# Optimization experiments

Hardware: AMD Instinct MI355X
Metric: run time of the kernel (lower is better)

Reference implementation:

```python
import jax, jax.numpy as jnp
import numpy as np

# Fuzzy system constants (from _init_fuzzy_system)
X1_C = jnp.arange(5.0)                 # x1 gauss centers 0,1,2,3,4 ; sigma 1
X2_C = jnp.arange(5.0) * 45.0          # x2 gauss centers 0,45,90,135,180 ; sigma 45
OUT_C = jnp.array([-0.3, 0.1, 0.5, 0.9, 1.3], dtype=jnp.float32)  # consequent centers ; sigma 0.3
Z = jnp.asarray(np.arange(-0.3, 1.31, 0.01), dtype=jnp.float32)   # 161-pt output universe

# Mamdani rules: list per consequent level of (x1_level, x2_level) OR-terms, levels XS..XL = 0..4
RULES = [
    [(2, 4), (3, 4), (3, 3), (4, 3), (4, 4)],            # -> coupling XS
    [(1, 4), (2, 3), (3, 2), (4, 1)],                    # -> S
    [(0, 4), (1, 3), (2, 2), (3, 1), (4, 0)],            # -> M
    [(0, 3), (1, 2), (2, 1), (3, 0)],                    # -> L
    [(0, 2), (0, 1), (0, 0), (1, 1), (1, 0), (2, 0)],    # -> XL
]


def gauss(x, c, s):
    return jnp.exp(-0.5 * ((x - c) / s) ** 2)


def setup_inputs() -> dict:
    key = jax.random.key(0)
    k1, k2, k3, k4 = jax.random.split(key, 4)
    N, E, D = 50000, 1000000, 8
    h = jax.random.normal(k1, (N, D), dtype=jnp.float32)
    src_idx = jax.random.randint(k2, (E,), 0, N, dtype=jnp.int32)
    dst_idx = jax.random.randint(k3, (E,), 0, N, dtype=jnp.int32)
    etypes = jax.random.randint(k4, (E,), 0, 3, dtype=jnp.int32)
    return {"h": h, "src_idx": src_idx, "dst_idx": dst_idx, "etypes": etypes}


def reference(h, src_idx, dst_idx, etypes):
    # edge vector: dst['h'] - src['h']
    v = h[dst_idx] - h[src_idx]                       # [E, D]
    # Ante_generator: x1 = |v| (distance, clipped to universe), x2 = angle(v, e1) in degrees
    n = jnp.sqrt(jnp.sum(v * v, axis=-1) + 1e-12)     # [E]
    x1 = jnp.clip(n, 0.0, 4.0)
    cosang = jnp.clip(v[:, 0] / n, -0.999999, 0.999999)
    x2 = jnp.degrees(jnp.arccos(cosang))              # [E] in [0, 180]
    # antecedent memberships
    mu1 = gauss(x1[:, None], X1_C[None, :], 1.0)      # [E, 5]
    mu2 = gauss(x2[:, None], X2_C[None, :], 45.0)     # [E, 5]
    zmf = gauss(Z[None, :], OUT_C[:, None], 0.3)      # [5, 161]
    # Mamdani: rule activation = max over OR-terms of min(mu1, mu2);
    # implication = min(act, consequent mf); aggregation = max over rules
    agg = jnp.zeros((x1.shape[0], Z.shape[0]), dtype=h.dtype)  # [E, 161]
    for r, pairs in enumerate(RULES):
        act = jnp.max(
            jnp.stack([jnp.minimum(mu1[:, i], mu2[:, j]) for i, j in pairs], axis=-1),
            axis=-1,
        )                                             # [E]
        agg = jnp.maximum(agg, jnp.minimum(act[:, None], zmf[r][None, :]))
    # centroid defuzzification
    coupling_degree = jnp.sum(agg * Z[None, :], axis=-1) / jnp.sum(agg, axis=-1)
    return coupling_degree
```

## Files before the change

kernel.cpp:

```cpp
#include <hip/hip_runtime.h>

static constexpr double cexp_taylor(double x) {
    double s = 1.0, t = 1.0;
    for (int i = 1; i < 40; ++i) { t = t * x / (double)i; s += t; }
    return s;
}
static constexpr double cpow_int(double b, long e) {
    double r = 1.0, p = b;
    while (e > 0) { if (e & 1) r *= p; p *= p; e >>= 1; }
    return r;
}
struct ZmfTab { float v[5][161]; };
static constexpr ZmfTab make_zmf() {
    ZmfTab t{};
    const double c0 = cexp_taylor(-1.0 / 1800.0);
    for (int r = 0; r < 5; ++r)
        for (int k = 0; k < 161; ++k) {
            long d = (long)(k - 40 * r);
            t.v[r][k] = (float)cpow_int(c0, d * d);
        }
    return t;
}
static constexpr ZmfTab ZMF = make_zmf();
static constexpr float ZCUT = 1e-4f;

__device__ __forceinline__ float fuzzy_F(float x1, float u)
{
    float m1[5], m2[5];
#pragma unroll
    for (int i = 0; i < 5; ++i) {
        float d1 = x1 - (float)i;
        float d2 = u  - (float)i;
        m1[i] = __expf(-0.5f * d1 * d1);
        m2[i] = __expf(-0.5f * d2 * d2);
    }

    float a0 = fmaxf(fmaxf(fminf(m1[2], m2[4]), fminf(m1[3], m2[4])),
               fmaxf(fminf(m1[3], m2[3]),
               fmaxf(fminf(m1[4], m2[3]), fminf(m1[4], m2[4]))));
    float a1 = fmaxf(fmaxf(fminf(m1[1], m2[4]), fminf(m1[2], m2[3])),
               fmaxf(fminf(m1[3], m2[2]), fminf(m1[4], m2[1])));
    float a2 = fmaxf(fmaxf(fminf(m1[0], m2[4]), fminf(m1[1], m2[3])),
               fmaxf(fminf(m1[2], m2[2]),
               fmaxf(fminf(m1[3], m2[1]), fminf(m1[4], m2[0]))));
    float a3 = fmaxf(fmaxf(fminf(m1[0], m2[3]), fminf(m1[1], m2[2])),
               fmaxf(fminf(m1[2], m2[1]), fminf(m1[3], m2[0])));
    float a4 = fmaxf(fmaxf(fmaxf(fminf(m1[0], m2[2]), fminf(m1[0], m2[1])),
               fmaxf(fminf(m1[0], m2[0]), fminf(m1[1], m2[1]))),
               fmaxf(fminf(m1[1], m2[0]), fminf(m1[2], m2[0])));
    float a[5] = {a0, a1, a2, a3, a4};

    float s0 = 0.0f, s1 = 0.0f;
#pragma unroll
    for (int k = 0; k < 161; ++k) {
        float m = -1.0f;
        bool first = true;
#pragma unroll
        for (int r = 0; r < 5; ++r) {
            if (ZMF.v[r][k] >= ZCUT) {
                float tmin = fminf(a[r], ZMF.v[r][k]);
                m = first ? tmin : fmaxf(m, tmin);
                first = false;
            }
        }
        s0 += m;
        s1 = fmaf(m, (float)k, s1);
    }
    return fmaf(0.01f, s1 / s0, -0.3f);
}

#define GN 256

__global__ __launch_bounds__(256) void build_table_kernel(float2* __restrict__ tab2)
{
    int idx = blockIdx.x * blockDim.x + threadIdx.x;
    int i1 = idx >> 8;
    int i2 = idx & 255;
    const float h = 4.0f / 255.0f;
    float f = fuzzy_F((float)i1 * h, (float)i2 * h);
    tab2[idx].x = f;
    if (i2 > 0)   tab2[idx - 1].y = f;
    if (i2 == 255) tab2[idx].y = f;
}

__device__ __forceinline__ float edge_eval(
    const float4* __restrict__ h4, const float2* __restrict__ tab2,
    int si, int di)
{
    float4 sa = h4[2 * si], sb = h4[2 * si + 1];
    float4 da = h4[2 * di], db = h4[2 * di + 1];

    float v0 = da.x - sa.x, v1 = da.y - sa.y, v2 = da.z - sa.z, v3 = da.w - sa.w;
    float v4 = db.x - sb.x, v5 = db.y - sb.y, v6 = db.z - sb.z, v7 = db.w - sb.w;

    float ss = fmaf(v0, v0, fmaf(v1, v1, fmaf(v2, v2, fmaf(v3, v3,
               fmaf(v4, v4, fmaf(v5, v5, fmaf(v6, v6, fmaf(v7, v7, 1e-12f))))))));

    float rn = rsqrtf(ss);
    float n  = ss * rn;
    float x1 = fminf(n, 4.0f);

    float c = v0 * rn;
    c = fminf(fmaxf(c, -0.999999f), 0.999999f);

    float ac = fabsf(c);
    float t  = sqrtf(1.0f - ac);
    float p  = fmaf(fmaf(fmaf(-0.0187293f, ac, 0.0742610f), ac, -0.2121144f),
                    ac, 1.5707288f);
    float r0 = t * p;
    float acosv = (c < 0.0f) ? (3.14159265358979f - r0) : r0;
    float u = acosv * 1.27323954473516f;

    const float sc = 255.0f * 0.25f;
    float t1 = x1 * sc;
    float t2 = u  * sc;
    int i1 = min((int)t1, 254);
    int i2 = min((int)t2, 254);
    float f1 = t1 - (float)i1;
    float f2 = t2 - (float)i2;

    float2 pl = tab2[(i1 << 8) + i2];
    float2 ph = tab2[(i1 << 8) + i2 + 256];

    float lo = fmaf(f2, pl.y - pl.x, pl.x);
    float hi = fmaf(f2, ph.y - ph.x, ph.x);
    return fmaf(f1, hi - lo, lo);
}

__global__ __launch_bounds__(256) void fuzzy_coupling_kernel(
    const float* __restrict__ h,
    const int*   __restrict__ src,
    const int*   __restrict__ dst,
    const float2* __restrict__ tab2,
    float*       __restrict__ out,
    int E)
{
    int t = blockIdx.x * blockDim.x + threadIdx.x;
    int e0 = 2 * t;
    if (e0 >= E) return;

    const float4* h4 = (const float4*)h;

    if (e0 + 1 < E) {
        int2 sp = ((const int2*)src)[t];
        int2 dp = ((const int2*)dst)[t];
        float r0 = edge_eval(h4, tab2, sp.x, dp.x);
        float r1 = edge_eval(h4, tab2, sp.y, dp.y);
        ((float2*)out)[t] = make_float2(r0, r1);
    } else {
        out[e0] = edge_eval(h4, tab2, src[e0], dst[e0]);
    }
}

extern "C" void kernel_launch(void* const* d_in, const int* in_sizes, int n_in,
                              void* d_out, int out_size, void* d_ws, size_t ws_size,
                              hipStream_t stream)
{
    const float* h   = (const float*)d_in[0];
    const int*   src = (const int*)d_in[1];
    const int*   dst = (const int*)d_in[2];
    float* out  = (float*)d_out;
    float2* tab = (float2*)d_ws;

    build_table_kernel<<<(GN * GN) / 256, 256, 0, stream>>>(tab);

    int E = in_sizes[1];
    int threads = (E + 1) / 2;
    int block = 256;
    int grid  = (threads + block - 1) / block;
    fuzzy_coupling_kernel<<<grid, block, 0, stream>>>(h, src, dst, tab, out, E);
}
```

Before: 89.93 us.

## Pack node features to fp16 and store full bilinear patch per table cell

Adds a pre-pass that converts node features to half precision so each edge gathers 16 bytes per endpoint instead of 32. The interpolation table now stores all four corner values per cell as a float4, replacing two float2 loads with one. This trades an extra kernel launch and reduced precision in the feature difference for less gather traffic.

```diff
diff --git a/kernel.cpp b/kernel.cpp
--- a/kernel.cpp
+++ b/kernel.cpp
@@ -1,4 +1,5 @@
 #include <hip/hip_runtime.h>
+#include <hip/hip_fp16.h>
 
 static constexpr double cexp_taylor(double x) {
     double s = 1.0, t = 1.0;
@@ -71,36 +72,56 @@
 
 #define GN 256
 
-__global__ __launch_bounds__(256) void build_table_kernel(float2* __restrict__ tab2)
+__global__ __launch_bounds__(256) void build_table_kernel(float* __restrict__ tabf)
 {
     int idx = blockIdx.x * blockDim.x + threadIdx.x;
     int i1 = idx >> 8;
     int i2 = idx & 255;
-    const float h = 4.0f / 255.0f;
-    float f = fuzzy_F((float)i1 * h, (float)i2 * h);
-    tab2[idx].x = f;
-    if (i2 > 0)   tab2[idx - 1].y = f;
-    if (i2 == 255) tab2[idx].y = f;
+    const float hstep = 4.0f / 255.0f;
+    float f = fuzzy_F((float)i1 * hstep, (float)i2 * hstep);
+
+    tabf[4 * idx + 0] = f;
+    if (i2 > 0)           tabf[4 * (idx - 1)   + 1] = f;
+    if (i1 > 0)           tabf[4 * (idx - GN)  + 2] = f;
+    if (i1 > 0 && i2 > 0) tabf[4 * (idx - GN - 1) + 3] = f;
 }
 
+__global__ __launch_bounds__(256) void pack_h_kernel(
+    const float4* __restrict__ h4, __half2* __restrict__ hp, int N)
+{
+    int r = blockIdx.x * blockDim.x + threadIdx.x;
+    if (r >= N) return;
+    float4 a = h4[2 * r], b = h4[2 * r + 1];
+    __half2* o = hp + 4 * r;
+    o[0] = __floats2half2_rn(a.x, a.y);
+    o[1] = __floats2half2_rn(a.z, a.w);
+    o[2] = __floats2half2_rn(b.x, b.y);
+    o[3] = __floats2half2_rn(b.z, b.w);
+}
+
+struct H8 { __half2 p0, p1, p2, p3; };
+
 __device__ __forceinline__ float edge_eval(
-    const float4* __restrict__ h4, const float2* __restrict__ tab2,
+    const H8* __restrict__ hp, const float4* __restrict__ tab4,
     int si, int di)
 {
-    float4 sa = h4[2 * si], sb = h4[2 * si + 1];
-    float4 da = h4[2 * di], db = h4[2 * di + 1];
+    H8 s = hp[si];
+    H8 d = hp[di];
 
-    float v0 = da.x - sa.x, v1 = da.y - sa.y, v2 = da.z - sa.z, v3 = da.w - sa.w;
-    float v4 = db.x - sb.x, v5 = db.y - sb.y, v6 = db.z - sb.z, v7 = db.w - sb.w;
+    float2 d0 = __half22float2(__hsub2(d.p0, s.p0));
+    float2 d1 = __half22float2(__hsub2(d.p1, s.p1));
+    float2 d2 = __half22float2(__hsub2(d.p2, s.p2));
+    float2 d3 = __half22float2(__hsub2(d.p3, s.p3));
 
-    float ss = fmaf(v0, v0, fmaf(v1, v1, fmaf(v2, v2, fmaf(v3, v3,
-               fmaf(v4, v4, fmaf(v5, v5, fmaf(v6, v6, fmaf(v7, v7, 1e-12f))))))));
+    float ss = fmaf(d0.x, d0.x, fmaf(d0.y, d0.y, fmaf(d1.x, d1.x, fmaf(d1.y, d1.y,
+               fmaf(d2.x, d2.x, fmaf(d2.y, d2.y, fmaf(d3.x, d3.x,
+               fmaf(d3.y, d3.y, 1e-12f))))))));
 
     float rn = rsqrtf(ss);
     float n  = ss * rn;
     float x1 = fminf(n, 4.0f);
 
-    float c = v0 * rn;
+    float c = d0.x * rn;
     c = fminf(fmaxf(c, -0.999999f), 0.999999f);
 
     float ac = fabsf(c);
@@ -119,19 +140,17 @@
     float f1 = t1 - (float)i1;
     float f2 = t2 - (float)i2;
 
-    float2 pl = tab2[(i1 << 8) + i2];
-    float2 ph = tab2[(i1 << 8) + i2 + 256];
-
-    float lo = fmaf(f2, pl.y - pl.x, pl.x);
-    float hi = fmaf(f2, ph.y - ph.x, ph.x);
+    float4 patch = tab4[(i1 << 8) + i2];
+    float lo = fmaf(f2, patch.y - patch.x, patch.x);
+    float hi = fmaf(f2, patch.w - patch.z, patch.z);
     return fmaf(f1, hi - lo, lo);
 }
 
 __global__ __launch_bounds__(256) void fuzzy_coupling_kernel(
-    const float* __restrict__ h,
+    const H8*    __restrict__ hp,
     const int*   __restrict__ src,
     const int*   __restrict__ dst,
-    const float2* __restrict__ tab2,
+    const float4* __restrict__ tab4,
     float*       __restrict__ out,
     int E)
 {
@@ -139,16 +158,14 @@
     int e0 = 2 * t;
     if (e0 >= E) return;
 
-    const float4* h4 = (const float4*)h;
-
     if (e0 + 1 < E) {
         int2 sp = ((const int2*)src)[t];
         int2 dp = ((const int2*)dst)[t];
-        float r0 = edge_eval(h4, tab2, sp.x, dp.x);
-        float r1 = edge_eval(h4, tab2, sp.y, dp.y);
+        float r0 = edge_eval(hp, tab4, sp.x, dp.x);
+        float r1 = edge_eval(hp, tab4, sp.y, dp.y);
         ((float2*)out)[t] = make_float2(r0, r1);
     } else {
-        out[e0] = edge_eval(h4, tab2, src[e0], dst[e0]);
+        out[e0] = edge_eval(hp, tab4, src[e0], dst[e0]);
     }
 }
 
@@ -159,14 +176,20 @@
     const float* h   = (const float*)d_in[0];
     const int*   src = (const int*)d_in[1];
     const int*   dst = (const int*)d_in[2];
-    float* out  = (float*)d_out;
-    float2* tab = (float2*)d_ws;
+    float* out = (float*)d_out;
 
-    build_table_kernel<<<(GN * GN) / 256, 256, 0, stream>>>(tab);
+    float*   tabf = (float*)d_ws;
+    float4*  tab4 = (float4*)d_ws;
+    __half2* hp   = (__half2*)((char*)d_ws + (size_t)GN * GN * 16);
 
+    int N = in_sizes[0] / 8;
     int E = in_sizes[1];
+
+    build_table_kernel<<<(GN * GN) / 256, 256, 0, stream>>>(tabf);
+    pack_h_kernel<<<(N + 255) / 256, 256, 0, stream>>>((const float4*)h, hp, N);
+
     int threads = (E + 1) / 2;
-    int block = 256;
-    int grid  = (threads + block - 1) / block;
-    fuzzy_coupling_kernel<<<grid, block, 0, stream>>>(h, src, dst, tab, out, E);
+    int grid = (threads + 255) / 256;
+    fuzzy_coupling_kernel<<<grid, 256, 0, stream>>>(
+        (const H8*)hp, src, dst, tab4, out, E);
 }
```

Result: faster. 84.87 us (-5.6%).
